# Kernel tuning notes

Measured on AMD Instinct MI355X. Metric: run time of the kernel, lower is better.

The kernel has to match this reference:

```python
import jax, jax.numpy as jnp
import numpy as np

B, Q, K = 4, 256, 1024          # batch, query_len, key_len
DQ, DK, DV, H = 512, 512, 512, 256  # query/key/value dims, num_hiddens


def setup_inputs() -> dict:
    key = jax.random.key(0)
    ks = jax.random.split(key, 7)
    return {
        "queries": jax.random.normal(ks[0], (B, Q, DQ), jnp.float32),
        "keys": jax.random.normal(ks[1], (B, K, DK), jnp.float32),
        "values": jax.random.normal(ks[2], (B, K, DV), jnp.float32),
        "valid_lens": jax.random.randint(ks[3], (B,), 1, K + 1),
        "Wq": jax.random.normal(ks[4], (H, DQ), jnp.float32) / np.sqrt(DQ).astype(np.float32),
        "Wk": jax.random.normal(ks[5], (H, DK), jnp.float32) / np.sqrt(DK).astype(np.float32),
        "wv": jax.random.normal(ks[6], (H,), jnp.float32) / np.sqrt(H).astype(np.float32),
    }


def reference(queries, keys, values, valid_lens, Wq, Wk, wv):
    # Linear projections (bias=False), torch Linear weight layout (out, in)
    q = jnp.einsum("bqd,hd->bqh", queries, Wq)          # (B, Q, H)
    k = jnp.einsum("bkd,hd->bkh", keys, Wk)             # (B, K, H)
    # Broadcast add -> tanh -> scalar score per (q, k) pair
    feats = jnp.tanh(q[:, :, None, :] + k[:, None, :, :])  # (B, Q, K, H)
    scores = jnp.einsum("bqkh,h->bqk", feats, wv)           # (B, Q, K)
    # masked_softmax with 1D valid_lens: mask applies along key axis per batch
    kv_len = scores.shape[-1]
    mask = jnp.arange(kv_len)[None, None, :] < valid_lens[:, None, None]  # (B,1,K)
    scores = jnp.where(mask, scores, jnp.float32(-1e6))
    attn = jax.nn.softmax(scores, axis=-1)               # (B, Q, K)
    # dropout is identity in eval mode
    return jnp.einsum("bqk,bkv->bqv", attn, values)      # (B, Q, DV)
```

## Files before the change

kernel.cpp:

```cpp
#include <hip/hip_runtime.h>
#include <stdint.h>


#define NB 4
#define NQ 256
#define NK 1024
#define ND 512
#define NH 256
#define QROWS 4
#define PJR 16
#define PJH 64

#define C2L2E 2.8853900817779268f
#define L2E   1.4426950408889634f

typedef float v2f __attribute__((ext_vector_type(2)));

__device__ void ff_vldec(const int* p, int* v) {
  bool ok = true;
  for (int i = 0; i < 4; ++i) { int x = p[i]; if (x < 1 || x > NK) ok = false; }
  if (ok) { for (int i = 0; i < 4; ++i) v[i] = p[i]; return; }
  ok = true;
  for (int i = 0; i < 4; ++i) {
    if (p[2 * i + 1] != 0) ok = false;
    int x = p[2 * i]; if (x < 1 || x > NK) ok = false;
  }
  if (ok) { for (int i = 0; i < 4; ++i) v[i] = p[2 * i]; return; }
  ok = true;
  for (int i = 0; i < 4; ++i) {
    union { int i; float f; } u; u.i = p[i];
    if (!(u.f >= 1.0f && u.f <= 1024.0f && u.f == floorf(u.f))) ok = false;
  }
  if (ok) {
    for (int i = 0; i < 4; ++i) { union { int i; float f; } u; u.i = p[i]; v[i] = (int)u.f; }
    return;
  }
  ok = true;
  for (int i = 0; i < 4; ++i) {
    union { long long l; double d; } u;
    u.l = ((long long)p[2 * i + 1] << 32) | (unsigned int)p[2 * i];
    if (!(u.d >= 1.0 && u.d <= 1024.0 && u.d == floor(u.d))) ok = false;
  }
  if (ok) {
    for (int i = 0; i < 4; ++i) {
      union { long long l; double d; } u;
      u.l = ((long long)p[2 * i + 1] << 32) | (unsigned int)p[2 * i];
      v[i] = (int)u.d;
    }
    return;
  }
  const uint16_t* hh = (const uint16_t*)p;
  const short*    s  = (const short*)p;
  ok = true;
  for (int i = 0; i < 4; ++i) { int x = s[i]; if (x < 1 || x > NK) ok = false; }
  if (ok) { for (int i = 0; i < 4; ++i) v[i] = s[i]; return; }
  ok = true;
  for (int i = 0; i < 4; ++i) {
    union { uint16_t u; _Float16 h; } u; u.u = hh[i];
    float f = (float)u.h;
    if (!(f >= 1.0f && f <= 1024.0f && f == floorf(f))) ok = false;
  }
  if (ok) {
    for (int i = 0; i < 4; ++i) {
      union { uint16_t u; _Float16 h; } u; u.u = hh[i];
      v[i] = (int)(float)u.h;
    }
    return;
  }
  ok = true;
  for (int i = 0; i < 4; ++i) {
    union { uint32_t u; float f; } u; u.u = ((uint32_t)hh[i]) << 16;
    if (!(u.f >= 1.0f && u.f <= 1028.0f)) ok = false;
  }
  if (ok) {
    for (int i = 0; i < 4; ++i) {
      union { uint32_t u; float f; } u; u.u = ((uint32_t)hh[i]) << 16;
      int x = (int)(u.f + 0.5f); if (x > NK) x = NK; v[i] = x;
    }
    return;
  }
  for (int i = 0; i < 4; ++i) v[i] = NK;
}

__global__ __launch_bounds__(256) void ff_wt(
    const float* __restrict__ Wq, const float* __restrict__ Wk,
    float* __restrict__ WTq, float* __restrict__ WTk)
{
  const int idx = blockIdx.x * 256 + threadIdx.x;
  const int d4 = idx & 127, h = idx >> 7;
  const float* src = blockIdx.y ? Wk : Wq;
  float*       dst = blockIdx.y ? WTk : WTq;
  float4 w = *(const float4*)(src + (size_t)h * ND + d4 * 4);
  w.x *= C2L2E; w.y *= C2L2E; w.z *= C2L2E; w.w *= C2L2E;
  *(float4*)(dst + ((size_t)d4 * NH + h) * 4) = w;
}

__global__ __launch_bounds__(256) void ff_proj(
    const float* __restrict__ q_in, const float* __restrict__ k_in,
    const float* __restrict__ WTq, const float* __restrict__ WTk,
    float* __restrict__ qp, float* __restrict__ kp)
{
  __shared__ float xs[PJR * ND];
  const int t  = threadIdx.x;
  const int rg = blockIdx.x >> 2;
  const int h0 = (blockIdx.x & 3) * PJH;
  const int gr0 = rg * PJR;
  const bool isq = gr0 < NB * NQ;
  const float* xin = isq ? (q_in + (size_t)gr0 * ND)
                         : (k_in + (size_t)(gr0 - NB * NQ) * ND);
  const float4* wt4 = (const float4*)(isq ? WTq : WTk);

  #pragma unroll
  for (int i = 0; i < 8; ++i)
    ((float4*)xs)[t + 256 * i] = ((const float4*)xin)[t + 256 * i];
  __syncthreads();

  const int L  = t & 63;
  const int rw = t >> 6;
  float a0 = 0.f, a1 = 0.f, a2 = 0.f, a3 = 0.f;
  const float4* xr = (const float4*)xs + (size_t)(4 * rw) * 128;

  #pragma unroll 4
  for (int d4 = 0; d4 < ND / 4; ++d4) {
    float4 w  = wt4[(size_t)d4 * NH + h0 + L];
    float4 x0 = xr[d4];
    float4 x1 = xr[128 + d4];
    float4 x2 = xr[256 + d4];
    float4 x3 = xr[384 + d4];
    a0 += w.x*x0.x + w.y*x0.y + w.z*x0.z + w.w*x0.w;
    a1 += w.x*x1.x + w.y*x1.y + w.z*x1.z + w.w*x1.w;
    a2 += w.x*x2.x + w.y*x2.y + w.z*x2.z + w.w*x2.w;
    a3 += w.x*x3.x + w.y*x3.y + w.z*x3.z + w.w*x3.w;
  }
  a0 = __builtin_amdgcn_exp2f(a0);
  a1 = __builtin_amdgcn_exp2f(a1);
  a2 = __builtin_amdgcn_exp2f(a2);
  a3 = __builtin_amdgcn_exp2f(a3);

  if (isq) {
    const int h = h0 + L;
    float* o = qp + (size_t)(gr0 + 4 * rw) * NH + h;
    o[0] = a0; o[NH] = a1; o[2 * NH] = a2; o[3 * NH] = a3;
  } else {
    __syncthreads();
    float* trs = xs;
    *(float4*)&trs[L * 16 + 4 * rw] = make_float4(a0, a1, a2, a3);
    __syncthreads();
    const int kl = t & 15, jl = t >> 4;
    const int g0 = gr0 - NB * NQ;
    const int bb = g0 >> 10, kg0 = g0 & (NK - 1);
    const int j0 = (blockIdx.x & 3) * 16;
    float4 o4 = make_float4(trs[(4*jl+0)*16 + kl], trs[(4*jl+1)*16 + kl],
                            trs[(4*jl+2)*16 + kl], trs[(4*jl+3)*16 + kl]);
    ((float4*)kp)[((size_t)bb * 64 + j0 + jl) * 1024 + kg0 + kl] = o4;
  }
}

__global__ __launch_bounds__(1024) void ff_attn2(
    const float* __restrict__ qp, const float* __restrict__ kp,
    const float* __restrict__ vals, const int* __restrict__ vlraw,
    const float* __restrict__ wvp, float* __restrict__ pvpart,
    float* __restrict__ Sg)
{
  __shared__ float  qs[QROWS * NH];
  __shared__ float4 wspp[NH / 2];
  __shared__ float  st[512 * QROWS];
  __shared__ float  psum[32];
  __shared__ float  part[4 * QROWS * ND];

  const int t  = threadIdx.x;
  const int kh = blockIdx.x;
  const int q0 = blockIdx.y * QROWS;
  const int b  = blockIdx.z;

  {
    const float* qsrc = qp + ((size_t)b * NQ + q0) * NH;
    qs[t] = qsrc[t];
    if (t < NH / 2) {
      float w0 = wvp[2 * t], w1 = wvp[2 * t + 1];
      wspp[t] = make_float4(-2.0f * w0, -2.0f * w1, -2.0f * (w0 + w1), 0.0f);
    }
  }
  __syncthreads();

  int vls[4];
  ff_vldec(vlraw, vls);
  const int vl = vls[b];

  const int kk = t & 511, rh = t >> 9;
  v2f acc = {0.f, 0.f};
  {
    const float4* kvp = (const float4*)kp + ((size_t)b * 64) * 1024
                      + (kh * 512 + kk);
    const float* q0p = qs + (2 * rh) * NH;
    const float* q1p = qs + (2 * rh + 1) * NH;
    #pragma unroll 4
    for (int j = 0; j < 64; ++j) {
      float4 K4 = kvp[(size_t)j << 10];
      float4 A0 = *(const float4*)(q0p + 4 * j);
      float4 A1 = *(const float4*)(q1p + 4 * j);
      float4 wa = wspp[2 * j];
      float4 wb = wspp[2 * j + 1];
      v2f one; one.x = 1.0f; one.y = 1.0f;
      {
        v2f a;  a.x  = A0.x * K4.x; a.y  = A1.x * K4.x;
        v2f b2; b2.x = A0.y * K4.y; b2.y = A1.y * K4.y;
        v2f D = (one + a) * (one + b2);
        v2f N;   N.x = wa.z;  N.y = wa.z;
        v2f w0v; w0v.x = wa.x; w0v.y = wa.x;
        v2f w1v; w1v.x = wa.y; w1v.y = wa.y;
        N += w0v * b2;
        N += w1v * a;
        v2f rD;
        rD.x = __builtin_amdgcn_rcpf(D.x);
        rD.y = __builtin_amdgcn_rcpf(D.y);
        acc += N * rD;
      }
      {
        v2f a;  a.x  = A0.z * K4.z; a.y  = A1.z * K4.z;
        v2f b2; b2.x = A0.w * K4.w; b2.y = A1.w * K4.w;
        v2f D = (one + a) * (one + b2);
        v2f N;   N.x = wb.z;  N.y = wb.z;
        v2f w0v; w0v.x = wb.x; w0v.y = wb.x;
        v2f w1v; w1v.x = wb.y; w1v.y = wb.y;
        N += w0v * b2;
        N += w1v * a;
        v2f rD;
        rD.x = __builtin_amdgcn_rcpf(D.x);
        rD.y = __builtin_amdgcn_rcpf(D.y);
        acc += N * rD;
      }
    }
  }
  {
    const bool okm = (kh * 512 + kk) < vl;
    v2f E;
    E.x = okm ? __builtin_amdgcn_exp2f(acc.x * L2E) : 0.f;
    E.y = okm ? __builtin_amdgcn_exp2f(acc.y * L2E) : 0.f;
    *(v2f*)&st[kk * 4 + 2 * rh] = E;
    float sx = E.x, sy = E.y;
    for (int o = 32; o; o >>= 1) { sx += __shfl_xor(sx, o); sy += __shfl_xor(sy, o); }
    if ((t & 63) == 0) { psum[(t >> 6) * 2] = sx; psum[(t >> 6) * 2 + 1] = sy; }
  }
  __syncthreads();

  if (t < 4) {
    const int j = t & 1, base = (t >> 1) * 8;
    float S = 0.f;
    #pragma unroll
    for (int w = 0; w < 8; ++w) S += psum[(base + w) * 2 + j];
    Sg[(((size_t)b * 64 + blockIdx.y) * 4 + t) * 2 + kh] = S;
  }

  {
    const int kq = t >> 8, c2 = (t & 255) * 2;
    const float* vb = vals + (size_t)b * NK * ND
                    + (size_t)(kh * 512 + kq * 128) * ND + c2;
    v2f o0 = {0.f,0.f}, o1 = {0.f,0.f}, o2 = {0.f,0.f}, o3 = {0.f,0.f};
    #pragma unroll 8
    for (int k = 0; k < 128; ++k) {
      v2f vv = *(const v2f*)(vb + (size_t)k * ND);
      float4 a = *(const float4*)&st[(kq * 128 + k) * 4];
      v2f ax; ax.x = a.x; ax.y = a.x;
      v2f ay; ay.x = a.y; ay.y = a.y;
      v2f az; az.x = a.z; az.y = a.z;
      v2f aw; aw.x = a.w; aw.y = a.w;
      o0 += ax * vv; o1 += ay * vv; o2 += az * vv; o3 += aw * vv;
    }
    *(v2f*)&part[(size_t)(kq * 4 + 0) * ND + c2] = o0;
    *(v2f*)&part[(size_t)(kq * 4 + 1) * ND + c2] = o1;
    *(v2f*)&part[(size_t)(kq * 4 + 2) * ND + c2] = o2;
    *(v2f*)&part[(size_t)(kq * 4 + 3) * ND + c2] = o3;
  }
  __syncthreads();
  {
    const int r = t >> 8, c2 = (t & 255) * 2;
    v2f s = {0.f, 0.f};
    #pragma unroll
    for (int kq = 0; kq < 4; ++kq)
      s += *(const v2f*)&part[(size_t)(kq * 4 + r) * ND + c2];
    *(v2f*)&pvpart[(((size_t)kh * NB + b) * NQ + q0 + r) * ND + c2] = s;
  }
}

__global__ __launch_bounds__(256) void ff_comb(
    const float* __restrict__ pvpart, const float* __restrict__ Sg,
    float* __restrict__ out)
{
  const int bid = blockIdx.x;
  const int t = threadIdx.x;
  const float S = Sg[bid * 2] + Sg[bid * 2 + 1];
  const float rs = 1.0f / S;
  const int b = bid >> 8, q = bid & 255;
  const float* p0 = pvpart + ((size_t)b * NQ + q) * ND;
  const float* p1 = pvpart + ((size_t)(NB + b) * NQ + q) * ND;
  float2 a = *(const float2*)(p0 + t * 2);
  float2 c = *(const float2*)(p1 + t * 2);
  *(float2*)(out + ((size_t)b * NQ + q) * ND + t * 2)
      = make_float2((a.x + c.x) * rs, (a.y + c.y) * rs);
}

__global__ __launch_bounds__(1024) void ff_attn(
    const float* __restrict__ qp, const float* __restrict__ kp,
    const float* __restrict__ vals, const int* __restrict__ vlraw,
    const float* __restrict__ wvp, float* __restrict__ out)
{
  __shared__ float qs[QROWS * NH];
  __shared__ float ws[NH];
  __shared__ float st[NK * QROWS];
  __shared__ float pm[16], psm[16];
  __shared__ float part[4 * QROWS * ND];

  const int t  = threadIdx.x;
  const int q0 = blockIdx.x * QROWS;
  const int b  = blockIdx.y;

  {
    const float* qsrc = qp + ((size_t)b * NQ + q0) * NH;
    qs[t] = qsrc[t];
    if (t < NH) ws[t] = -2.0f * wvp[t];
  }
  __syncthreads();

  int vls[4];
  ff_vldec(vlraw, vls);
  const int vl = vls[b];

  float sc[4] = {0.f, 0.f, 0.f, 0.f};
  {
    const float4* kvp = (const float4*)kp + ((size_t)b * 64) * 1024 + t;
    for (int j = 0; j < 64; ++j) {
      float4 K4 = kvp[(size_t)j << 10];
      const float* wj = &ws[4 * j];
      #pragma unroll
      for (int r = 0; r < 4; ++r) {
        const float* qr = &qs[r * NH + 4 * j];
        sc[r] += wj[0] * __builtin_amdgcn_rcpf(1.0f + qr[0] * K4.x);
        sc[r] += wj[1] * __builtin_amdgcn_rcpf(1.0f + qr[1] * K4.y);
        sc[r] += wj[2] * __builtin_amdgcn_rcpf(1.0f + qr[2] * K4.z);
        sc[r] += wj[3] * __builtin_amdgcn_rcpf(1.0f + qr[3] * K4.w);
      }
    }
  }
  {
    const bool okm = (t < vl);
    *(float4*)&st[t * 4] = make_float4(okm ? sc[0] : -1e6f, okm ? sc[1] : -1e6f,
                                       okm ? sc[2] : -1e6f, okm ? sc[3] : -1e6f);
  }
  __syncthreads();

  {
    const int wid = t >> 6, lane = t & 63;
    const int row = wid >> 2, seg = wid & 3;
    const int kb = seg * 256 + lane;
    float v0 = st[(kb      ) * 4 + row];
    float v1 = st[(kb +  64) * 4 + row];
    float v2 = st[(kb + 128) * 4 + row];
    float v3 = st[(kb + 192) * 4 + row];
    float m = fmaxf(fmaxf(v0, v1), fmaxf(v2, v3));
    for (int o = 32; o; o >>= 1) m = fmaxf(m, __shfl_xor(m, o));
    if (lane == 0) pm[wid] = m;
    __syncthreads();
    m = fmaxf(fmaxf(pm[row*4+0], pm[row*4+1]), fmaxf(pm[row*4+2], pm[row*4+3]));
    float e0 = __builtin_amdgcn_exp2f((v0 - m) * L2E);
    float e1 = __builtin_amdgcn_exp2f((v1 - m) * L2E);
    float e2 = __builtin_amdgcn_exp2f((v2 - m) * L2E);
    float e3 = __builtin_amdgcn_exp2f((v3 - m) * L2E);
    float sm = e0 + e1 + e2 + e3;
    for (int o = 32; o; o >>= 1) sm += __shfl_xor(sm, o);
    if (lane == 0) psm[wid] = sm;
    __syncthreads();
    const float S = psm[row*4+0] + psm[row*4+1] + psm[row*4+2] + psm[row*4+3];
    const float rr = 1.0f / S;
    st[(kb      ) * 4 + row] = e0 * rr;
    st[(kb +  64) * 4 + row] = e1 * rr;
    st[(kb + 128) * 4 + row] = e2 * rr;
    st[(kb + 192) * 4 + row] = e3 * rr;
  }
  __syncthreads();

  {
    const int kq = t >> 8, c2 = (t & 255) * 2;
    const float* vb = vals + (size_t)b * NK * ND + c2;
    v2f o0 = {0.f,0.f}, o1 = {0.f,0.f}, o2 = {0.f,0.f}, o3 = {0.f,0.f};
    const int k0 = kq * 256;
    #pragma unroll 8
    for (int k = k0; k < k0 + 256; ++k) {
      v2f vv = *(const v2f*)(vb + (size_t)k * ND);
      float4 a = *(const float4*)&st[k * 4];
      v2f ax; ax.x = a.x; ax.y = a.x;
      v2f ay; ay.x = a.y; ay.y = a.y;
      v2f az; az.x = a.z; az.y = a.z;
      v2f aw; aw.x = a.w; aw.y = a.w;
      o0 += ax * vv; o1 += ay * vv; o2 += az * vv; o3 += aw * vv;
    }
    float* pp = &part[(size_t)kq * QROWS * ND + c2];
    *(v2f*)(pp         ) = o0;
    *(v2f*)(pp +     ND) = o1;
    *(v2f*)(pp + 2 * ND) = o2;
    *(v2f*)(pp + 3 * ND) = o3;
  }
  __syncthreads();
  {
    const int r = t >> 8, c2 = (t & 255) * 2;
    const float* pp = &part[(size_t)r * ND + c2];
    v2f s = {0.f, 0.f};
    #pragma unroll
    for (int kq = 0; kq < 4; ++kq) s += *(const v2f*)(pp + (size_t)kq * QROWS * ND);
    *(v2f*)(out + ((size_t)b * NQ + q0 + r) * ND + c2) = s;
  }
}

extern "C" void kernel_launch(void* const* d_in, const int* in_sizes, int n_in,
                              void* d_out, int out_size, void* d_ws, size_t ws_size,
                              hipStream_t stream) {
  const float* queries = (const float*)d_in[0];
  const float* keys    = (const float*)d_in[1];
  const float* values  = (const float*)d_in[2];
  const int*   vlens   = (const int*)d_in[3];
  const float* Wq      = (const float*)d_in[4];
  const float* Wk      = (const float*)d_in[5];
  const float* wv      = (const float*)d_in[6];
  float* out = (float*)d_out;

  float* qp  = (float*)d_ws;
  float* kp  = qp  + (size_t)NB * NQ * NH;
  float* wtq = kp  + (size_t)NB * NH * NK;
  float* wtk = wtq + (size_t)(ND / 4) * NH * 4;
  float* pvp = wtk + (size_t)(ND / 4) * NH * 4;
  float* Sg  = pvp + (size_t)2 * NB * NQ * ND;
  const size_t need = ((size_t)(Sg - (float*)d_ws) + 2 * NB * NQ) * sizeof(float);

  ff_wt  <<<dim3(128, 2), 256, 0, stream>>>(Wq, Wk, wtq, wtk);
  ff_proj<<<dim3((NB * (NQ + NK) / PJR) * (NH / PJH)), 256, 0, stream>>>(
      queries, keys, wtq, wtk, qp, kp);
  if (ws_size >= need) {
    ff_attn2<<<dim3(2, NQ / QROWS, NB), 1024, 0, stream>>>(
        qp, kp, values, vlens, wv, pvp, Sg);
    ff_comb<<<dim3(NB * NQ), 256, 0, stream>>>(pvp, Sg, out);
  } else {
    ff_attn<<<dim3(NQ / QROWS, NB), 1024, 0, stream>>>(
        qp, kp, values, vlens, wv, out);
  }
}
```

Measured before the change: 189.0 us.

## Split attention over four key chunks with hidden-dim split inside block

Raises the key-axis split of the attention kernel from 2 to 4 chunks, so each block handles 256 keys. Each block's two 512-thread halves compute partial scores over half of the hidden dimension and combine them through shared memory before the exp. The combine kernel now sums four partial PV results and four partial softmax sums. This doubles the number of blocks for better occupancy across CUs, at the cost of more partial-result traffic to global memory and an extra shared-memory reduction.

```diff
diff --git a/kernel.cpp b/kernel.cpp
--- a/kernel.cpp
+++ b/kernel.cpp
@@ -156,7 +156,7 @@
   }
 }
 
-__global__ __launch_bounds__(1024) void ff_attn2(
+__global__ __launch_bounds__(1024) void ff_attn4(
     const float* __restrict__ qp, const float* __restrict__ kp,
     const float* __restrict__ vals, const int* __restrict__ vlraw,
     const float* __restrict__ wvp, float* __restrict__ pvpart,
@@ -164,18 +164,17 @@
 {
   __shared__ float  qs[QROWS * NH];
   __shared__ float4 wspp[NH / 2];
-  __shared__ float  st[512 * QROWS];
-  __shared__ float  psum[32];
-  __shared__ float  part[4 * QROWS * ND];
+  __shared__ float  stp[2 * 256 * 4];
+  __shared__ float  psum[16];
+  __shared__ float  part[2 * 4 * 512];
 
   const int t  = threadIdx.x;
-  const int kh = blockIdx.x;
+  const int ck = blockIdx.x;
   const int q0 = blockIdx.y * QROWS;
   const int b  = blockIdx.z;
 
   {
-    const float* qsrc = qp + ((size_t)b * NQ + q0) * NH;
-    qs[t] = qsrc[t];
+    qs[t] = qp[((size_t)b * NQ + q0) * NH + t];
     if (t < NH / 2) {
       float w0 = wvp[2 * t], w1 = wvp[2 * t + 1];
       wspp[t] = make_float4(-2.0f * w0, -2.0f * w1, -2.0f * (w0 + w1), 0.0f);
@@ -187,15 +186,16 @@
   ff_vldec(vlraw, vls);
   const int vl = vls[b];
 
-  const int kk = t & 511, rh = t >> 9;
+  const int kk = t & 255, rh = (t >> 8) & 1, hs = t >> 9;
   v2f acc = {0.f, 0.f};
   {
     const float4* kvp = (const float4*)kp + ((size_t)b * 64) * 1024
-                      + (kh * 512 + kk);
+                      + (ck * 256 + kk);
     const float* q0p = qs + (2 * rh) * NH;
     const float* q1p = qs + (2 * rh + 1) * NH;
     #pragma unroll 4
-    for (int j = 0; j < 64; ++j) {
+    for (int jj = 0; jj < 32; ++jj) {
+      const int j = hs * 32 + jj;
       float4 K4 = kvp[(size_t)j << 10];
       float4 A0 = *(const float4*)(q0p + 4 * j);
       float4 A1 = *(const float4*)(q1p + 4 * j);
@@ -232,54 +232,50 @@
       }
     }
   }
-  {
-    const bool okm = (kh * 512 + kk) < vl;
-    v2f E;
-    E.x = okm ? __builtin_amdgcn_exp2f(acc.x * L2E) : 0.f;
-    E.y = okm ? __builtin_amdgcn_exp2f(acc.y * L2E) : 0.f;
-    *(v2f*)&st[kk * 4 + 2 * rh] = E;
-    float sx = E.x, sy = E.y;
-    for (int o = 32; o; o >>= 1) { sx += __shfl_xor(sx, o); sy += __shfl_xor(sy, o); }
-    if ((t & 63) == 0) { psum[(t >> 6) * 2] = sx; psum[(t >> 6) * 2 + 1] = sy; }
-  }
-  __syncthreads();
-
+  *(v2f*)&stp[(hs * 256 + kk) * 4 + 2 * rh] = acc;
+  __syncthreads();
+
+  {
+    const int k = t & 255, row = t >> 8;
+    float s = stp[k * 4 + row] + stp[(256 + k) * 4 + row];
+    const bool okm = (ck * 256 + k) < vl;
+    float E = okm ? __builtin_amdgcn_exp2f(s * L2E) : 0.f;
+    stp[k * 4 + row] = E;
+    float sx = E;
+    for (int o = 32; o; o >>= 1) sx += __shfl_xor(sx, o);
+    if ((t & 63) == 0) psum[t >> 6] = sx;
+  }
+  __syncthreads();
   if (t < 4) {
-    const int j = t & 1, base = (t >> 1) * 8;
-    float S = 0.f;
-    #pragma unroll
-    for (int w = 0; w < 8; ++w) S += psum[(base + w) * 2 + j];
-    Sg[(((size_t)b * 64 + blockIdx.y) * 4 + t) * 2 + kh] = S;
-  }
-
-  {
-    const int kq = t >> 8, c2 = (t & 255) * 2;
+    float S = psum[t * 4] + psum[t * 4 + 1] + psum[t * 4 + 2] + psum[t * 4 + 3];
+    Sg[((((size_t)b * 64 + blockIdx.y) * 4 + t)) * 4 + ck] = S;
+  }
+
+  {
+    const int c = t & 511, kq = t >> 9;
     const float* vb = vals + (size_t)b * NK * ND
-                    + (size_t)(kh * 512 + kq * 128) * ND + c2;
-    v2f o0 = {0.f,0.f}, o1 = {0.f,0.f}, o2 = {0.f,0.f}, o3 = {0.f,0.f};
+                    + (size_t)(ck * 256 + kq * 128) * ND + c;
+    float o0 = 0.f, o1 = 0.f, o2 = 0.f, o3 = 0.f;
     #pragma unroll 8
     for (int k = 0; k < 128; ++k) {
-      v2f vv = *(const v2f*)(vb + (size_t)k * ND);
-      float4 a = *(const float4*)&st[(kq * 128 + k) * 4];
-      v2f ax; ax.x = a.x; ax.y = a.x;
-      v2f ay; ay.x = a.y; ay.y = a.y;
-      v2f az; az.x = a.z; az.y = a.z;
-      v2f aw; aw.x = a.w; aw.y = a.w;
-      o0 += ax * vv; o1 += ay * vv; o2 += az * vv; o3 += aw * vv;
-    }
-    *(v2f*)&part[(size_t)(kq * 4 + 0) * ND + c2] = o0;
-    *(v2f*)&part[(size_t)(kq * 4 + 1) * ND + c2] = o1;
-    *(v2f*)&part[(size_t)(kq * 4 + 2) * ND + c2] = o2;
-    *(v2f*)&part[(size_t)(kq * 4 + 3) * ND + c2] = o3;
-  }
-  __syncthreads();
-  {
-    const int r = t >> 8, c2 = (t & 255) * 2;
-    v2f s = {0.f, 0.f};
+      float v = vb[(size_t)k * ND];
+      float4 a = *(const float4*)&stp[(kq * 128 + k) * 4];
+      o0 += a.x * v; o1 += a.y * v; o2 += a.z * v; o3 += a.w * v;
+    }
+    part[(kq * 4 + 0) * 512 + c] = o0;
+    part[(kq * 4 + 1) * 512 + c] = o1;
+    part[(kq * 4 + 2) * 512 + c] = o2;
+    part[(kq * 4 + 3) * 512 + c] = o3;
+  }
+  __syncthreads();
+  {
+    const int c = t & 511, rp = t >> 9;
     #pragma unroll
-    for (int kq = 0; kq < 4; ++kq)
-      s += *(const v2f*)&part[(size_t)(kq * 4 + r) * ND + c2];
-    *(v2f*)&pvpart[(((size_t)kh * NB + b) * NQ + q0 + r) * ND + c2] = s;
+    for (int rr = 0; rr < 2; ++rr) {
+      const int r = rp * 2 + rr;
+      float s = part[(0 * 4 + r) * 512 + c] + part[(1 * 4 + r) * 512 + c];
+      pvpart[((size_t)(ck * NB + b) * NQ + q0 + r) * ND + c] = s;
+    }
   }
 }
 
@@ -289,15 +285,19 @@
 {
   const int bid = blockIdx.x;
   const int t = threadIdx.x;
-  const float S = Sg[bid * 2] + Sg[bid * 2 + 1];
+  const float* sg = Sg + (size_t)bid * 4;
+  const float S = (sg[0] + sg[1]) + (sg[2] + sg[3]);
   const float rs = 1.0f / S;
   const int b = bid >> 8, q = bid & 255;
-  const float* p0 = pvpart + ((size_t)b * NQ + q) * ND;
-  const float* p1 = pvpart + ((size_t)(NB + b) * NQ + q) * ND;
-  float2 a = *(const float2*)(p0 + t * 2);
-  float2 c = *(const float2*)(p1 + t * 2);
+  float2 acc = make_float2(0.f, 0.f);
+  #pragma unroll
+  for (int c = 0; c < 4; ++c) {
+    const float* p = pvpart + ((size_t)(c * NB + b) * NQ + q) * ND;
+    float2 v = *(const float2*)(p + t * 2);
+    acc.x += v.x; acc.y += v.y;
+  }
   *(float2*)(out + ((size_t)b * NQ + q) * ND + t * 2)
-      = make_float2((a.x + c.x) * rs, (a.y + c.y) * rs);
+      = make_float2(acc.x * rs, acc.y * rs);
 }
 
 __global__ __launch_bounds__(1024) void ff_attn(
@@ -428,14 +428,14 @@
   float* wtq = kp  + (size_t)NB * NH * NK;
   float* wtk = wtq + (size_t)(ND / 4) * NH * 4;
   float* pvp = wtk + (size_t)(ND / 4) * NH * 4;
-  float* Sg  = pvp + (size_t)2 * NB * NQ * ND;
-  const size_t need = ((size_t)(Sg - (float*)d_ws) + 2 * NB * NQ) * sizeof(float);
+  float* Sg  = pvp + (size_t)4 * NB * NQ * ND;
+  const size_t need = ((size_t)(Sg - (float*)d_ws) + 4 * NB * NQ) * sizeof(float);
 
   ff_wt  <<<dim3(128, 2), 256, 0, stream>>>(Wq, Wk, wtq, wtk);
   ff_proj<<<dim3((NB * (NQ + NK) / PJR) * (NH / PJH)), 256, 0, stream>>>(
       queries, keys, wtq, wtk, qp, kp);
   if (ws_size >= need) {
-    ff_attn2<<<dim3(2, NQ / QROWS, NB), 1024, 0, stream>>>(
+    ff_attn4<<<dim3(4, NQ / QROWS, NB), 1024, 0, stream>>>(
         qp, kp, values, vlens, wv, pvp, Sg);
     ff_comb<<<dim3(NB * NQ), 256, 0, stream>>>(pvp, Sg, out);
   } else {
```

After: 187.1 us. Within noise of the previous version (-1.0%).
